# Kernel optimization log

Measured on AMD Instinct MI355X. Metric: run time of the kernel, lower is better.

Reference implementation:

```python
import jax, jax.numpy as jnp
import numpy as np

S, D, H, FF = 2048, 1024, 16, 4096
DH = D // H
EPS = 1e-5


def gelu(x):
    return 0.5 * x * (1 + jnp.tanh(jnp.sqrt(2 / jnp.pi) * (x + 0.044715 * jnp.power(x, 3))))


def layer_norm(x, w, b):
    mu = jnp.mean(x, axis=-1, keepdims=True)
    var = jnp.mean(jnp.square(x - mu), axis=-1, keepdims=True)
    return (x - mu) * jnp.power(var + EPS, -0.5) * w + b


def glorot(key, shape):
    fan_in, fan_out = shape[0], shape[1]
    lim = jnp.sqrt(6.0 / (fan_in + fan_out))
    return jax.random.uniform(key, shape, jnp.float32, -lim, lim)


def setup_inputs() -> dict:
    key = jax.random.key(0)
    ks = jax.random.split(key, 6)
    return {
        "x": jax.random.normal(ks[0], (S, D), jnp.float32),
        "W_qkv": glorot(ks[1], (D, 3 * D)),
        "W_o": glorot(ks[2], (D, D)),
        "W1": glorot(ks[3], (D, FF)),
        "b1": jnp.zeros((FF,), jnp.float32),
        "W2": glorot(ks[4], (FF, D)),
        "b2": jnp.zeros((D,), jnp.float32),
        "ln_att_w": jnp.ones((D,), jnp.float32),
        "ln_att_b": jnp.zeros((D,), jnp.float32),
        "ln_mlp_w": jnp.ones((D,), jnp.float32),
        "ln_mlp_b": jnp.zeros((D,), jnp.float32),
    }


def attention(x, W_qkv, W_o):
    qkv = (x @ W_qkv).reshape(S, 3, H, DH)
    q, k, v = qkv[:, 0], qkv[:, 1], qkv[:, 2]  # each [S, H, DH]
    # scores [H, S_q, S_k]
    scores = jnp.einsum("qhd,khd->hqk", q, k) / jnp.sqrt(jnp.float32(DH))
    causal = jnp.tril(jnp.ones((S, S), bool))
    scores = jnp.where(causal[None], scores, -jnp.inf)
    w = jax.nn.softmax(scores, axis=2)
    out = jnp.einsum("hqk,khd->qhd", w, v).reshape(S, D)
    return out @ W_o


def reference(x, W_qkv, W_o, W1, b1, W2, b2, ln_att_w, ln_att_b, ln_mlp_w, ln_mlp_b):
    x = x + attention(layer_norm(x, ln_att_w, ln_att_b), W_qkv, W_o)
    h = layer_norm(x, ln_mlp_w, ln_mlp_b)
    mlp_out = gelu(h @ W1 + b1) @ W2 + b2
    return x + mlp_out
```

## Files before the change

### kernel.cpp

```cpp
#include <hip/hip_runtime.h>
#include <math.h>

typedef __bf16 bf16;
typedef __bf16 bf16x4 __attribute__((ext_vector_type(4)));
typedef __bf16 bf16x8 __attribute__((ext_vector_type(8)));
typedef float f32x4 __attribute__((ext_vector_type(4)));
typedef unsigned short u16;
typedef unsigned short u16x8 __attribute__((ext_vector_type(8)));
typedef unsigned int u32;

__device__ __forceinline__ u16 f2bf(float f) {
  union { float f; u32 u; } v; v.f = f;
  u32 u = v.u;
  return (u16)((u + 0x7FFFu + ((u >> 16) & 1u)) >> 16);
}

__device__ __forceinline__ f32x4 mfma16(bf16x8 a, bf16x8 b, f32x4 c) {
  return __builtin_amdgcn_mfma_f32_16x16x32_bf16(a, b, c, 0, 0, 0);
}

__device__ __forceinline__ void gld16(const void* g, void* l) {
  __builtin_amdgcn_global_load_lds(
      (const __attribute__((address_space(1))) void*)(void*)g,
      (__attribute__((address_space(3))) void*)l,
      16, 0, 0);
}

__device__ __forceinline__ void wconv_body(const float* __restrict__ W,
                                           u16* __restrict__ Wt, int K, int N,
                                           int bx, int by) {
  __shared__ float tile[64][65];
  const int k0 = by * 64, n0 = bx * 64;
  const int t = threadIdx.x;
  const int tr = t >> 4;
  const int tc = (t & 15) * 4;
#pragma unroll
  for (int it = 0; it < 4; it++) {
    const int r = tr + it * 16;
    const float4 v = *(const float4*)(W + (size_t)(k0 + r) * N + n0 + tc);
    tile[r][tc] = v.x; tile[r][tc + 1] = v.y; tile[r][tc + 2] = v.z; tile[r][tc + 3] = v.w;
  }
  __syncthreads();
#pragma unroll
  for (int it = 0; it < 4; it++) {
    const int rn = tr + it * 16;
    ushort4 o;
    o.x = f2bf(tile[tc][rn]);
    o.y = f2bf(tile[tc + 1][rn]);
    o.z = f2bf(tile[tc + 2][rn]);
    o.w = f2bf(tile[tc + 3][rn]);
    *(ushort4*)(Wt + (size_t)(n0 + rn) * K + k0 + tc) = o;
  }
}

__global__ __launch_bounds__(256)
void wconv_all(const float* __restrict__ Wqkv, const float* __restrict__ Wo,
               const float* __restrict__ W1, const float* __restrict__ W2,
               u16* __restrict__ Wqkv_t, u16* __restrict__ Wo_t,
               u16* __restrict__ W1_t, u16* __restrict__ W2_t) {
  const int id = blockIdx.x;
  if (id < 768)       { wconv_body(Wqkv, Wqkv_t, 1024, 3072, id % 48, id / 48); }
  else if (id < 1024) { const int j = id - 768;  wconv_body(Wo, Wo_t, 1024, 1024, j % 16, j / 16); }
  else if (id < 2048) { const int j = id - 1024; wconv_body(W1, W1_t, 1024, 4096, j % 64, j / 64); }
  else                { const int j = id - 2048; wconv_body(W2, W2_t, 4096, 1024, j % 16, j / 16); }
}

__global__ __launch_bounds__(256)
void ln_bf16(const float* __restrict__ x, const float* __restrict__ w,
             const float* __restrict__ b, u16* __restrict__ out) {
  const int row = blockIdx.x;
  const int t = threadIdx.x;
  const float4 v = *(const float4*)(x + (size_t)row * 1024 + t * 4);
  float s = v.x + v.y + v.z + v.w;
  float s2 = v.x * v.x + v.y * v.y + v.z * v.z + v.w * v.w;
#pragma unroll
  for (int m = 1; m < 64; m <<= 1) {
    s += __shfl_xor(s, m);
    s2 += __shfl_xor(s2, m);
  }
  __shared__ float red[8];
  if ((t & 63) == 0) { red[t >> 6] = s; red[4 + (t >> 6)] = s2; }
  __syncthreads();
  s = red[0] + red[1] + red[2] + red[3];
  s2 = red[4] + red[5] + red[6] + red[7];
  const float mu = s * (1.f / 1024.f);
  const float var = fmaxf(s2 * (1.f / 1024.f) - mu * mu, 0.f);
  const float rstd = rsqrtf(var + 1e-5f);
  const float* wp = w + t * 4;
  const float* bp = b + t * 4;
  ushort4 o;
  o.x = f2bf((v.x - mu) * rstd * wp[0] + bp[0]);
  o.y = f2bf((v.y - mu) * rstd * wp[1] + bp[1]);
  o.z = f2bf((v.z - mu) * rstd * wp[2] + bp[2]);
  o.w = f2bf((v.w - mu) * rstd * wp[3] + bp[3]);
  *(ushort4*)(out + (size_t)row * 1024 + t * 4) = o;
}

__global__ __launch_bounds__(256)
void reduce_ln(const float* __restrict__ x, const float* __restrict__ p0,
               const float* __restrict__ p1, const float* __restrict__ w,
               const float* __restrict__ b, float* __restrict__ x2,
               u16* __restrict__ h2) {
  const int row = blockIdx.x;
  const int t = threadIdx.x;
  const size_t base = (size_t)row * 1024 + t * 4;
  float4 v = *(const float4*)(x + base);
  const float4 a = *(const float4*)(p0 + base);
  const float4 c = *(const float4*)(p1 + base);
  v.x += a.x + c.x; v.y += a.y + c.y; v.z += a.z + c.z; v.w += a.w + c.w;
  *(float4*)(x2 + base) = v;
  float s = v.x + v.y + v.z + v.w;
  float s2 = v.x * v.x + v.y * v.y + v.z * v.z + v.w * v.w;
#pragma unroll
  for (int m = 1; m < 64; m <<= 1) {
    s += __shfl_xor(s, m);
    s2 += __shfl_xor(s2, m);
  }
  __shared__ float red[8];
  if ((t & 63) == 0) { red[t >> 6] = s; red[4 + (t >> 6)] = s2; }
  __syncthreads();
  s = red[0] + red[1] + red[2] + red[3];
  s2 = red[4] + red[5] + red[6] + red[7];
  const float mu = s * (1.f / 1024.f);
  const float var = fmaxf(s2 * (1.f / 1024.f) - mu * mu, 0.f);
  const float rstd = rsqrtf(var + 1e-5f);
  const float* wp = w + t * 4;
  const float* bp = b + t * 4;
  ushort4 o;
  o.x = f2bf((v.x - mu) * rstd * wp[0] + bp[0]);
  o.y = f2bf((v.y - mu) * rstd * wp[1] + bp[1]);
  o.z = f2bf((v.z - mu) * rstd * wp[2] + bp[2]);
  o.w = f2bf((v.w - mu) * rstd * wp[3] + bp[3]);
  *(ushort4*)(h2 + base) = o;
}

__global__ __launch_bounds__(256)
void reduce_out(const float* __restrict__ x2, const float* __restrict__ bias,
                const float* __restrict__ p0, const float* __restrict__ p1,
                float* __restrict__ out) {
  const size_t base = ((size_t)blockIdx.x * 256 + threadIdx.x) * 4;
  const int col = (int)(base & 1023);
  float4 v = *(const float4*)(x2 + base);
  const float4 a = *(const float4*)(p0 + base);
  const float4 c = *(const float4*)(p1 + base);
  const float4 bb = *(const float4*)(bias + col);
  v.x += a.x + c.x + bb.x;
  v.y += a.y + c.y + bb.y;
  v.z += a.z + c.z + bb.z;
  v.w += a.w + c.w + bb.w;
  *(float4*)(out + base) = v;
}

template <int BM, int BN, int EPI, int KS>
__global__ __launch_bounds__(256)
void gemm_bf16(const u16* __restrict__ A, const u16* __restrict__ Bt,
               int M, int N, int K,
               const float* __restrict__ bias,
               float* __restrict__ po0, float* __restrict__ po1,
               u16* __restrict__ outB,
               u16* __restrict__ qo, u16* __restrict__ ko, u16* __restrict__ vo) {
  constexpr int ASZ = BM * 32;
  constexpr int BSZ = BN * 32;
  constexpr int NLD = (BM == 128 ? 2 : 1) + (BN == 128 ? 2 : 1);
  __shared__ __attribute__((aligned(16))) u16 lA[2 * ASZ];
  __shared__ __attribute__((aligned(16))) u16 lB[2 * BSZ];
  const int t = threadIdx.x;
  const int l = t & 63;
  const int w = t >> 6;
  constexpr int NJ = (BM == 128 && BN == 128) ? 4 : 2;
  const int WR = (BM == 128) ? (w >> 1) * 64 : 0;
  const int WC = (BM == 128) ? ((BN == 128) ? (w & 1) * 64 : (w & 1) * 32)
                             : w * 32;
  const int l15 = l & 15, lg = l >> 4;

  const int nx = gridDim.x;
  const u32 bid = blockIdx.y * nx + blockIdx.x;
  const int nxc = nx >> 3;
  const u32 r = bid >> 3;
  const int bx = (bid & 7) * nxc + (int)(r % (u32)nxc);
  const int by = (int)(r / (u32)nxc);

  const int m0 = by * BM, n0 = bx * BN;
  const int KC = K / KS;
  const int kbase = blockIdx.z * KC;

  f32x4 acc[4][NJ] = {};

  const int lr = t >> 2;
  const int lc = ((t & 3) << 3) + kbase;
  const u16* ag0 = A + (size_t)(m0 + lr) * K + lc;
  const u16* ag1 = A + (size_t)(m0 + 64 + lr) * K + lc;
  const u16* bg0 = Bt + (size_t)(n0 + lr) * K + lc;
  const u16* bg1 = Bt + (size_t)(n0 + 64 + lr) * K + lc;

  const int nt = KC / 32;
  auto stage = [&](int buf, int kt) {
    const int k0 = kt * 32;
    gld16(ag0 + k0, &lA[buf * ASZ + t * 8]);
    if (BM == 128) gld16(ag1 + k0, &lA[buf * ASZ + 2048 + t * 8]);
    gld16(bg0 + k0, &lB[buf * BSZ + t * 8]);
    if (BN == 128) gld16(bg1 + k0, &lB[buf * BSZ + 2048 + t * 8]);
  };

  stage(0, 0);

  for (int kt = 0; kt < nt; kt++) {
    const int cur = kt & 1;
    if (kt + 1 < nt) {
      stage(cur ^ 1, kt + 1);
      if constexpr (NLD == 4) {
        asm volatile("s_waitcnt vmcnt(4)" ::: "memory");
      } else {
        asm volatile("s_waitcnt vmcnt(3)" ::: "memory");
      }
    } else {
      asm volatile("s_waitcnt vmcnt(0)" ::: "memory");
    }
    __builtin_amdgcn_s_barrier();
    bf16x8 af[4], bfr[NJ];
#pragma unroll
    for (int i = 0; i < 4; i++)
      af[i] = *(const bf16x8*)&lA[cur * ASZ + (WR + i * 16 + l15) * 32 + lg * 8];
#pragma unroll
    for (int j = 0; j < NJ; j++)
      bfr[j] = *(const bf16x8*)&lB[cur * BSZ + (WC + j * 16 + l15) * 32 + lg * 8];
    asm volatile("s_waitcnt lgkmcnt(0)" ::: "memory");
    __builtin_amdgcn_s_barrier();
    __builtin_amdgcn_sched_barrier(0);
#pragma unroll
    for (int i = 0; i < 4; i++)
#pragma unroll
      for (int j = 0; j < NJ; j++)
        acc[i][j] = mfma16(af[i], bfr[j], acc[i][j]);
  }

  float* po = (KS == 2 && blockIdx.z == 1) ? po1 : po0;
  const int mr0 = m0 + WR + lg * 4;
  const int nc0 = n0 + WC + l15;
#pragma unroll
  for (int i = 0; i < 4; i++) {
    const int mr = mr0 + i * 16;
#pragma unroll
    for (int j = 0; j < NJ; j++) {
      const int nc = nc0 + j * 16;
      if (EPI == 0) {
        const int sel = nc >> 10;
        const int d = nc & 1023;
        const int h = d >> 6, dl = d & 63;
        const int kt2 = mr >> 5;
        if (sel == 2) {
          const int lgp = (mr >> 3) & 3, el0 = mr & 7;
          const int nb = dl >> 4, l15p = dl & 15;
          u16* dst = vo + (size_t)(h * 64 + kt2) * 2048 + nb * 512 +
                     (lgp * 16 + l15p) * 8 + el0;
          ushort4 o;
          o.x = f2bf(acc[i][j][0]); o.y = f2bf(acc[i][j][1]);
          o.z = f2bf(acc[i][j][2]); o.w = f2bf(acc[i][j][3]);
          *(ushort4*)dst = o;
        } else {
          const int f = (mr >> 4) & 1, l15p0 = mr & 15;
          const int kk = dl >> 5, lgp = (dl >> 3) & 3, el = dl & 7;
          u16* dst = (sel == 0 ? qo : ko) + (size_t)(h * 64 + kt2) * 2048 +
                     f * 1024 + kk * 512 + (lgp * 16 + l15p0) * 8 + el;
#pragma unroll
          for (int e = 0; e < 4; e++)
            dst[e * 8] = f2bf(acc[i][j][e]);
        }
      } else if (EPI == 2) {
        const float bb = bias[nc];
#pragma unroll
        for (int e = 0; e < 4; e++) {
          const float v = acc[i][j][e] + bb;
          const float g = 0.5f * v * (1.0f + tanhf(0.7978845608028654f * (v + 0.044715f * v * v * v)));
          outB[(size_t)(mr + e) * N + nc] = f2bf(g);
        }
      } else {
#pragma unroll
        for (int e = 0; e < 4; e++)
          po[(size_t)(mr + e) * N + nc] = acc[i][j][e];
      }
    }
  }
}

__device__ __forceinline__ void attn_load(
    bf16x8 (&kf)[2][2], bf16x8 (&vf)[4],
    const u16* __restrict__ Kp, const u16* __restrict__ Vp,
    int hkt, int l) {
#pragma unroll
  for (int f = 0; f < 2; f++)
#pragma unroll
    for (int kk = 0; kk < 2; kk++)
      kf[kk][f] = *(const bf16x8*)(Kp + hkt + f * 1024 + kk * 512 + l * 8);
#pragma unroll
  for (int nb = 0; nb < 4; nb++)
    vf[nb] = *(const bf16x8*)(Vp + hkt + nb * 512 + l * 8);
}

__device__ __forceinline__ void attn_tile(
    const bf16x8 (&kf)[2][2], const bf16x8 (&vf)[4], const bf16x8 (&qf)[2][2],
    f32x4 (&accO)[2][4], float (&lsum)[2], u16* myP,
    int k0, bool diag, int qb, int l15, int lg) {
  f32x4 sv[2][2] = {};
  __builtin_amdgcn_s_setprio(1);
#pragma unroll
  for (int g = 0; g < 2; g++)
#pragma unroll
    for (int f = 0; f < 2; f++)
#pragma unroll
      for (int kk = 0; kk < 2; kk++)
        sv[g][f] = mfma16(kf[kk][f], qf[g][kk], sv[g][f]);
  __builtin_amdgcn_s_setprio(0);
#pragma unroll
  for (int g = 0; g < 2; g++) {
#pragma unroll
    for (int f = 0; f < 2; f++) {
      bf16x4 pk;
      float ps = 0.f;
#pragma unroll
      for (int e = 0; e < 4; e++) {
        float p = exp2f(sv[g][f][e] * 0.1803368801f);
        if (diag && (k0 + f * 16 + lg * 4 + e > qb + g * 16 + l15)) p = 0.f;
        ps += p;
        pk[e] = (bf16)p;
      }
      lsum[g] += ps;
      *(bf16x4*)(myP + g * 640 + l15 * 40 + f * 16 + lg * 4) = pk;
    }
  }
  const bf16x8 pf0 = *(const bf16x8*)(myP + l15 * 40 + lg * 8);
  const bf16x8 pf1 = *(const bf16x8*)(myP + 640 + l15 * 40 + lg * 8);
  __builtin_amdgcn_s_setprio(1);
#pragma unroll
  for (int nb = 0; nb < 4; nb++) {
    accO[0][nb] = mfma16(pf0, vf[nb], accO[0][nb]);
    accO[1][nb] = mfma16(pf1, vf[nb], accO[1][nb]);
  }
  __builtin_amdgcn_s_setprio(0);
}

__global__ __launch_bounds__(256)
void attn_fwd(const u16* __restrict__ Qp, const u16* __restrict__ Kp,
              const u16* __restrict__ Vp, u16* __restrict__ Ob) {
  __shared__ __attribute__((aligned(16))) char smem[33280];
  float* sO = (float*)smem;
  float* sL = (float*)(smem + 32768);
  u16* lP = (u16*)smem;

  const int t = threadIdx.x;
  const int l = t & 63, w = t >> 6;
  const int l15 = l & 15, lg = l >> 4;
  const u32 bid = blockIdx.x;
  const u32 vb = (bid & 7) * 128 + (bid >> 3);
  const int h = (int)(vb >> 6);
  const int qt = 63 - (int)(vb & 63);
  const int qb = qt * 32;

  u16* myPA = lP + w * 1280;
  u16* myPB = lP + 5120 + w * 1280;

  bf16x8 qf[2][2];
#pragma unroll
  for (int g = 0; g < 2; g++)
#pragma unroll
    for (int kk = 0; kk < 2; kk++)
      qf[g][kk] = *(const bf16x8*)(Qp + (size_t)(h * 64 + qt) * 2048 +
                                   g * 1024 + kk * 512 + l * 8);

  f32x4 accO[2][4] = {};
  float lsum[2] = {0.f, 0.f};

  if (w <= qt) {
    const int hb = h * 64;
    bf16x8 kfA[2][2], vfA[4], kfB[2][2], vfB[4];
    attn_load(kfA, vfA, Kp, Vp, (hb + w) * 2048, l);
    int kt = w;
    while (true) {
      const int ktB = kt + 4;
      const bool hasB = (ktB <= qt);
      attn_load(kfB, vfB, Kp, Vp, (hb + (hasB ? ktB : kt)) * 2048, l);
      attn_tile(kfA, vfA, qf, accO, lsum, myPA, kt * 32, kt == qt, qb, l15, lg);
      if (!hasB) break;
      const int ktA = kt + 8;
      const bool hasA = (ktA <= qt);
      attn_load(kfA, vfA, Kp, Vp, (hb + (hasA ? ktA : ktB)) * 2048, l);
      attn_tile(kfB, vfB, qf, accO, lsum, myPB, ktB * 32, ktB == qt, qb, l15, lg);
      if (!hasA) break;
      kt = ktA;
    }
  }

  float lsr[2];
#pragma unroll
  for (int g = 0; g < 2; g++) {
    float v = lsum[g];
    v += __shfl_xor(v, 16);
    v += __shfl_xor(v, 32);
    lsr[g] = v;
  }

  __syncthreads();
#pragma unroll
  for (int g = 0; g < 2; g++) {
#pragma unroll
    for (int nb = 0; nb < 4; nb++)
#pragma unroll
      for (int e = 0; e < 4; e++)
        sO[w * 2048 + (g * 16 + lg * 4 + e) * 64 + nb * 16 + l15] = accO[g][nb][e];
    if (lg == 0) sL[w * 32 + g * 16 + l15] = lsr[g];
  }
  __syncthreads();

  const int base = t * 8;
  const int row = base >> 6;
  const int col = base & 63;
  f32x4 a0 = {}, a1 = {};
  float ls = 0.f;
#pragma unroll
  for (int ww = 0; ww < 4; ww++) {
    a0 += *(const f32x4*)&sO[ww * 2048 + base];
    a1 += *(const f32x4*)&sO[ww * 2048 + base + 4];
    ls += sL[ww * 32 + row];
  }
  const float rinv = 1.0f / ls;
  u16x8 o;
#pragma unroll
  for (int j = 0; j < 4; j++) {
    o[j] = f2bf(a0[j] * rinv);
    o[4 + j] = f2bf(a1[j] * rinv);
  }
  *(u16x8*)(Ob + (size_t)(qb + row) * 1024 + h * 64 + col) = o;
}

extern "C" void kernel_launch(void* const* d_in, const int* in_sizes, int n_in,
                              void* d_out, int out_size, void* d_ws, size_t ws_size,
                              hipStream_t stream) {
  const float* x     = (const float*)d_in[0];
  const float* W_qkv = (const float*)d_in[1];
  const float* W_o   = (const float*)d_in[2];
  const float* W1    = (const float*)d_in[3];
  const float* b1    = (const float*)d_in[4];
  const float* W2    = (const float*)d_in[5];
  const float* b2    = (const float*)d_in[6];
  const float* ln_aw = (const float*)d_in[7];
  const float* ln_ab = (const float*)d_in[8];
  const float* ln_mw = (const float*)d_in[9];
  const float* ln_mb = (const float*)d_in[10];

  char* ws = (char*)d_ws;
  u16* Wqkv_t = (u16*)(ws);
  u16* Wo_t   = (u16*)(ws + 6291456);
  u16* W1_t   = (u16*)(ws + 8388608);
  u16* W2_t   = (u16*)(ws + 16777216);
  u16* h1     = (u16*)(ws + 25165824);
  u16* h2     = h1;
  u16* Qp     = (u16*)(ws + 29360128);
  u16* Kp     = (u16*)(ws + 33554432);
  u16* Vp     = (u16*)(ws + 37748736);
  u16* attnb  = (u16*)(ws + 41943040);
  u16* ffb    = (u16*)(ws + 29360128);
  float* p0   = (float*)(ws + 46137344);
  float* p1   = (float*)(ws + 54525952);
  float* x2   = (float*)(ws + 62914560);
  (void)ws_size; (void)in_sizes; (void)n_in; (void)out_size;

  wconv_all<<<3072, 256, 0, stream>>>(W_qkv, W_o, W1, W2, Wqkv_t, Wo_t, W1_t, W2_t);

  ln_bf16<<<2048, 256, 0, stream>>>(x, ln_aw, ln_ab, h1);

  gemm_bf16<128, 128, 0, 1><<<dim3(24, 16), 256, 0, stream>>>(
      h1, Wqkv_t, 2048, 3072, 1024, nullptr, nullptr, nullptr, nullptr, Qp, Kp, Vp);

  attn_fwd<<<1024, 256, 0, stream>>>(Qp, Kp, Vp, attnb);

  gemm_bf16<64, 128, 4, 2><<<dim3(8, 32, 2), 256, 0, stream>>>(
      attnb, Wo_t, 2048, 1024, 1024, nullptr, p0, p1, nullptr, nullptr, nullptr, nullptr);

  reduce_ln<<<2048, 256, 0, stream>>>(x, p0, p1, ln_mw, ln_mb, x2, h2);

  gemm_bf16<128, 128, 2, 1><<<dim3(32, 16), 256, 0, stream>>>(
      h2, W1_t, 2048, 4096, 1024, b1, nullptr, nullptr, ffb, nullptr, nullptr, nullptr);

  gemm_bf16<64, 128, 4, 2><<<dim3(8, 32, 2), 256, 0, stream>>>(
      ffb, W2_t, 2048, 1024, 4096, nullptr, p0, p1, nullptr, nullptr, nullptr, nullptr);

  reduce_out<<<2048, 256, 0, stream>>>(x2, b2, p0, p1, (float*)d_out);
}
```

Before: 169.9 us.

## Deepen GEMM pipeline to a 4-slot LDS ring with register-double-buffered fragments

The bf16 GEMM main loop now uses a 4-slot shared-memory ring and prefetches global tiles two K-steps ahead instead of one. The MFMA operand fragments for the next step are loaded from LDS into a second register set while the current step's MFMAs run. This removes the second per-iteration barrier and the full lgkmcnt(0) stall before the MFMAs, so LDS reads and global loads can overlap with compute. In exchange it doubles LDS use per block, which may lower occupancy, and it adds fragment registers. The manual two-step unroll assumes an even number of K tiles.

```diff
diff --git a/kernel.cpp b/kernel.cpp
--- a/kernel.cpp
+++ b/kernel.cpp
@@ -162,12 +162,13 @@
   constexpr int ASZ = BM * 32;
   constexpr int BSZ = BN * 32;
   constexpr int NLD = (BM == 128 ? 2 : 1) + (BN == 128 ? 2 : 1);
-  __shared__ __attribute__((aligned(16))) u16 lA[2 * ASZ];
-  __shared__ __attribute__((aligned(16))) u16 lB[2 * BSZ];
+  constexpr int NJ = (BM == 128 && BN == 128) ? 4 : 2;
+  constexpr int NFR = 4 + NJ;
+  __shared__ __attribute__((aligned(16))) u16 lA[4 * ASZ];
+  __shared__ __attribute__((aligned(16))) u16 lB[4 * BSZ];
   const int t = threadIdx.x;
   const int l = t & 63;
   const int w = t >> 6;
-  constexpr int NJ = (BM == 128 && BN == 128) ? 4 : 2;
   const int WR = (BM == 128) ? (w >> 1) * 64 : 0;
   const int WC = (BM == 128) ? ((BN == 128) ? (w & 1) * 64 : (w & 1) * 32)
                              : w * 32;
@@ -201,37 +202,50 @@
     gld16(bg0 + k0, &lB[buf * BSZ + t * 8]);
     if (BN == 128) gld16(bg1 + k0, &lB[buf * BSZ + 2048 + t * 8]);
   };
-
-  stage(0, 0);
-
-  for (int kt = 0; kt < nt; kt++) {
-    const int cur = kt & 1;
-    if (kt + 1 < nt) {
-      stage(cur ^ 1, kt + 1);
-      if constexpr (NLD == 4) {
-        asm volatile("s_waitcnt vmcnt(4)" ::: "memory");
-      } else {
-        asm volatile("s_waitcnt vmcnt(3)" ::: "memory");
-      }
+  auto ldfrag = [&](int buf, bf16x8 (&af)[4], bf16x8 (&bf_)[NJ]) {
+#pragma unroll
+    for (int i = 0; i < 4; i++)
+      af[i] = *(const bf16x8*)&lA[buf * ASZ + (WR + i * 16 + l15) * 32 + lg * 8];
+#pragma unroll
+    for (int j = 0; j < NJ; j++)
+      bf_[j] = *(const bf16x8*)&lB[buf * BSZ + (WC + j * 16 + l15) * 32 + lg * 8];
+  };
+  auto body = [&](int ti, bf16x8 (&afc)[4], bf16x8 (&bfc)[NJ],
+                  bf16x8 (&afn)[4], bf16x8 (&bfn)[NJ]) {
+    if (ti + 2 < nt) {
+      stage((ti + 2) & 3, ti + 2);
+      if constexpr (NLD == 4) asm volatile("s_waitcnt vmcnt(4)" ::: "memory");
+      else                    asm volatile("s_waitcnt vmcnt(3)" ::: "memory");
     } else {
       asm volatile("s_waitcnt vmcnt(0)" ::: "memory");
     }
     __builtin_amdgcn_s_barrier();
-    bf16x8 af[4], bfr[NJ];
+    if (ti + 1 < nt) {
+      ldfrag((ti + 1) & 3, afn, bfn);
+      if constexpr (NFR == 8) asm volatile("s_waitcnt lgkmcnt(8)" ::: "memory");
+      else                    asm volatile("s_waitcnt lgkmcnt(6)" ::: "memory");
+    } else {
+      asm volatile("s_waitcnt lgkmcnt(0)" ::: "memory");
+    }
+    __builtin_amdgcn_sched_barrier(0);
 #pragma unroll
     for (int i = 0; i < 4; i++)
-      af[i] = *(const bf16x8*)&lA[cur * ASZ + (WR + i * 16 + l15) * 32 + lg * 8];
-#pragma unroll
-    for (int j = 0; j < NJ; j++)
-      bfr[j] = *(const bf16x8*)&lB[cur * BSZ + (WC + j * 16 + l15) * 32 + lg * 8];
-    asm volatile("s_waitcnt lgkmcnt(0)" ::: "memory");
-    __builtin_amdgcn_s_barrier();
-    __builtin_amdgcn_sched_barrier(0);
-#pragma unroll
-    for (int i = 0; i < 4; i++)
 #pragma unroll
       for (int j = 0; j < NJ; j++)
-        acc[i][j] = mfma16(af[i], bfr[j], acc[i][j]);
+        acc[i][j] = mfma16(afc[i], bfc[j], acc[i][j]);
+  };
+
+  stage(0, 0);
+  stage(1, 1);
+  if constexpr (NLD == 4) asm volatile("s_waitcnt vmcnt(4)" ::: "memory");
+  else                    asm volatile("s_waitcnt vmcnt(3)" ::: "memory");
+  __builtin_amdgcn_s_barrier();
+  bf16x8 afA[4], bfA[NJ], afB[4], bfB[NJ];
+  ldfrag(0, afA, bfA);
+
+  for (int ti = 0; ti < nt; ti += 2) {
+    body(ti, afA, bfA, afB, bfB);
+    body(ti + 1, afB, bfB, afA, bfA);
   }
 
   float* po = (KS == 2 && blockIdx.z == 1) ? po1 : po0;
```

Result: no change. 167.6 us (-1.4%).

## Pre-pack GEMM operands into MFMA fragment layout and load directly to registers

Applied to the files above, without the earlier changes.

All bf16 GEMM operands (weights, LN outputs, attention output, GELU output) are now written in a packed 16x32 fragment-tiled layout. The GEMM kernel then loads MFMA fragments straight from global memory into registers with register double-buffering, dropping the LDS staging and barriers. Wo and W2 GEMMs move to 128x128 tiles with split-K of 4, and their partial sums are stored as bf16 instead of fp32 to cut reduction traffic. This adds precision loss in the partials and relies on L2/cache for operand reuse, since there is no shared-memory reuse across waves.

```diff
diff --git a/kernel.cpp b/kernel.cpp
--- a/kernel.cpp
+++ b/kernel.cpp
@@ -14,16 +14,18 @@
   u32 u = v.u;
   return (u16)((u + 0x7FFFu + ((u >> 16) & 1u)) >> 16);
 }
+__device__ __forceinline__ float bf2f(u16 u) {
+  union { u32 u; float f; } v; v.u = (u32)u << 16;
+  return v.f;
+}
 
 __device__ __forceinline__ f32x4 mfma16(bf16x8 a, bf16x8 b, f32x4 c) {
   return __builtin_amdgcn_mfma_f32_16x16x32_bf16(a, b, c, 0, 0, 0);
 }
 
-__device__ __forceinline__ void gld16(const void* g, void* l) {
-  __builtin_amdgcn_global_load_lds(
-      (const __attribute__((address_space(1))) void*)(void*)g,
-      (__attribute__((address_space(3))) void*)l,
-      16, 0, 0);
+__device__ __forceinline__ size_t pk_addr(int r, int c, int C) {
+  return ((size_t)(r >> 4) * (C >> 5) + (c >> 5)) * 512 +
+         ((c >> 3) & 3) * 128 + (r & 15) * 8 + (c & 7);
 }
 
 __device__ __forceinline__ void wconv_body(const float* __restrict__ W,
@@ -44,12 +46,14 @@
 #pragma unroll
   for (int it = 0; it < 4; it++) {
     const int rn = tr + it * 16;
+    const int n = n0 + rn;
+    const int k = k0 + tc;
     ushort4 o;
     o.x = f2bf(tile[tc][rn]);
     o.y = f2bf(tile[tc + 1][rn]);
     o.z = f2bf(tile[tc + 2][rn]);
     o.w = f2bf(tile[tc + 3][rn]);
-    *(ushort4*)(Wt + (size_t)(n0 + rn) * K + k0 + tc) = o;
+    *(ushort4*)(Wt + pk_addr(n, k, K)) = o;
   }
 }
 
@@ -93,21 +97,22 @@
   o.y = f2bf((v.y - mu) * rstd * wp[1] + bp[1]);
   o.z = f2bf((v.z - mu) * rstd * wp[2] + bp[2]);
   o.w = f2bf((v.w - mu) * rstd * wp[3] + bp[3]);
-  *(ushort4*)(out + (size_t)row * 1024 + t * 4) = o;
-}
-
-__global__ __launch_bounds__(256)
-void reduce_ln(const float* __restrict__ x, const float* __restrict__ p0,
-               const float* __restrict__ p1, const float* __restrict__ w,
-               const float* __restrict__ b, float* __restrict__ x2,
-               u16* __restrict__ h2) {
+  *(ushort4*)(out + pk_addr(row, t * 4, 1024)) = o;
+}
+
+__global__ __launch_bounds__(256)
+void reduce_ln(const float* __restrict__ x, const u16* __restrict__ pb,
+               const float* __restrict__ w, const float* __restrict__ b,
+               float* __restrict__ x2, u16* __restrict__ h2) {
   const int row = blockIdx.x;
   const int t = threadIdx.x;
   const size_t base = (size_t)row * 1024 + t * 4;
   float4 v = *(const float4*)(x + base);
-  const float4 a = *(const float4*)(p0 + base);
-  const float4 c = *(const float4*)(p1 + base);
-  v.x += a.x + c.x; v.y += a.y + c.y; v.z += a.z + c.z; v.w += a.w + c.w;
+#pragma unroll
+  for (int z = 0; z < 4; z++) {
+    const ushort4 p = *(const ushort4*)(pb + (size_t)z * 2097152 + base);
+    v.x += bf2f(p.x); v.y += bf2f(p.y); v.z += bf2f(p.z); v.w += bf2f(p.w);
+  }
   *(float4*)(x2 + base) = v;
   float s = v.x + v.y + v.z + v.w;
   float s2 = v.x * v.x + v.y * v.y + v.z * v.z + v.w * v.w;
@@ -131,46 +136,36 @@
   o.y = f2bf((v.y - mu) * rstd * wp[1] + bp[1]);
   o.z = f2bf((v.z - mu) * rstd * wp[2] + bp[2]);
   o.w = f2bf((v.w - mu) * rstd * wp[3] + bp[3]);
-  *(ushort4*)(h2 + base) = o;
+  *(ushort4*)(h2 + pk_addr(row, t * 4, 1024)) = o;
 }
 
 __global__ __launch_bounds__(256)
 void reduce_out(const float* __restrict__ x2, const float* __restrict__ bias,
-                const float* __restrict__ p0, const float* __restrict__ p1,
-                float* __restrict__ out) {
+                const u16* __restrict__ pb, float* __restrict__ out) {
   const size_t base = ((size_t)blockIdx.x * 256 + threadIdx.x) * 4;
   const int col = (int)(base & 1023);
   float4 v = *(const float4*)(x2 + base);
-  const float4 a = *(const float4*)(p0 + base);
-  const float4 c = *(const float4*)(p1 + base);
   const float4 bb = *(const float4*)(bias + col);
-  v.x += a.x + c.x + bb.x;
-  v.y += a.y + c.y + bb.y;
-  v.z += a.z + c.z + bb.z;
-  v.w += a.w + c.w + bb.w;
+  v.x += bb.x; v.y += bb.y; v.z += bb.z; v.w += bb.w;
+#pragma unroll
+  for (int z = 0; z < 4; z++) {
+    const ushort4 p = *(const ushort4*)(pb + (size_t)z * 2097152 + base);
+    v.x += bf2f(p.x); v.y += bf2f(p.y); v.z += bf2f(p.z); v.w += bf2f(p.w);
+  }
   *(float4*)(out + base) = v;
 }
 
-template <int BM, int BN, int EPI, int KS>
-__global__ __launch_bounds__(256)
-void gemm_bf16(const u16* __restrict__ A, const u16* __restrict__ Bt,
-               int M, int N, int K,
-               const float* __restrict__ bias,
-               float* __restrict__ po0, float* __restrict__ po1,
-               u16* __restrict__ outB,
-               u16* __restrict__ qo, u16* __restrict__ ko, u16* __restrict__ vo) {
-  constexpr int ASZ = BM * 32;
-  constexpr int BSZ = BN * 32;
-  constexpr int NLD = (BM == 128 ? 2 : 1) + (BN == 128 ? 2 : 1);
-  __shared__ __attribute__((aligned(16))) u16 lA[2 * ASZ];
-  __shared__ __attribute__((aligned(16))) u16 lB[2 * BSZ];
+template <int EPI, int KS>
+__global__ __launch_bounds__(256)
+void gemm_pk(const u16* __restrict__ Ap, const u16* __restrict__ Bp,
+             int M, int N, int K,
+             const float* __restrict__ bias, u16* __restrict__ pb,
+             u16* __restrict__ outB,
+             u16* __restrict__ qo, u16* __restrict__ ko, u16* __restrict__ vo) {
   const int t = threadIdx.x;
   const int l = t & 63;
   const int w = t >> 6;
-  constexpr int NJ = (BM == 128 && BN == 128) ? 4 : 2;
-  const int WR = (BM == 128) ? (w >> 1) * 64 : 0;
-  const int WC = (BM == 128) ? ((BN == 128) ? (w & 1) * 64 : (w & 1) * 32)
-                             : w * 32;
+  const int WR = (w >> 1) * 64, WC = (w & 1) * 64;
   const int l15 = l & 15, lg = l >> 4;
 
   const int nx = gridDim.x;
@@ -180,68 +175,50 @@
   const int bx = (bid & 7) * nxc + (int)(r % (u32)nxc);
   const int by = (int)(r / (u32)nxc);
 
-  const int m0 = by * BM, n0 = bx * BN;
-  const int KC = K / KS;
-  const int kbase = blockIdx.z * KC;
-
-  f32x4 acc[4][NJ] = {};
-
-  const int lr = t >> 2;
-  const int lc = ((t & 3) << 3) + kbase;
-  const u16* ag0 = A + (size_t)(m0 + lr) * K + lc;
-  const u16* ag1 = A + (size_t)(m0 + 64 + lr) * K + lc;
-  const u16* bg0 = Bt + (size_t)(n0 + lr) * K + lc;
-  const u16* bg1 = Bt + (size_t)(n0 + 64 + lr) * K + lc;
-
-  const int nt = KC / 32;
-  auto stage = [&](int buf, int kt) {
-    const int k0 = kt * 32;
-    gld16(ag0 + k0, &lA[buf * ASZ + t * 8]);
-    if (BM == 128) gld16(ag1 + k0, &lA[buf * ASZ + 2048 + t * 8]);
-    gld16(bg0 + k0, &lB[buf * BSZ + t * 8]);
-    if (BN == 128) gld16(bg1 + k0, &lB[buf * BSZ + 2048 + t * 8]);
+  const int m0 = by * 128, n0 = bx * 128;
+  const int KT = K >> 5;
+  const int nt = (K / KS) >> 5;
+  const int t0 = blockIdx.z * nt;
+
+  const u16* aB = Ap + ((size_t)((m0 + WR) >> 4) * KT + t0) * 512 + l * 8;
+  const u16* bB = Bp + ((size_t)((n0 + WC) >> 4) * KT + t0) * 512 + l * 8;
+
+  f32x4 acc[4][4] = {};
+  bf16x8 a0[4], b0[4], a1[4], b1[4];
+
+  auto LD = [&](bf16x8 (&af)[4], bf16x8 (&bf_)[4], int ti) {
+#pragma unroll
+    for (int i = 0; i < 4; i++)
+      af[i] = *(const bf16x8*)(aB + ((size_t)i * KT + ti) * 512);
+#pragma unroll
+    for (int j = 0; j < 4; j++)
+      bf_[j] = *(const bf16x8*)(bB + ((size_t)j * KT + ti) * 512);
   };
-
-  stage(0, 0);
-
-  for (int kt = 0; kt < nt; kt++) {
-    const int cur = kt & 1;
-    if (kt + 1 < nt) {
-      stage(cur ^ 1, kt + 1);
-      if constexpr (NLD == 4) {
-        asm volatile("s_waitcnt vmcnt(4)" ::: "memory");
-      } else {
-        asm volatile("s_waitcnt vmcnt(3)" ::: "memory");
-      }
-    } else {
-      asm volatile("s_waitcnt vmcnt(0)" ::: "memory");
-    }
-    __builtin_amdgcn_s_barrier();
-    bf16x8 af[4], bfr[NJ];
+  auto FMA = [&](bf16x8 (&af)[4], bf16x8 (&bf_)[4]) {
+    __builtin_amdgcn_s_setprio(1);
 #pragma unroll
     for (int i = 0; i < 4; i++)
-      af[i] = *(const bf16x8*)&lA[cur * ASZ + (WR + i * 16 + l15) * 32 + lg * 8];
-#pragma unroll
-    for (int j = 0; j < NJ; j++)
-      bfr[j] = *(const bf16x8*)&lB[cur * BSZ + (WC + j * 16 + l15) * 32 + lg * 8];
-    asm volatile("s_waitcnt lgkmcnt(0)" ::: "memory");
-    __builtin_amdgcn_s_barrier();
-    __builtin_amdgcn_sched_barrier(0);
-#pragma unroll
-    for (int i = 0; i < 4; i++)
-#pragma unroll
-      for (int j = 0; j < NJ; j++)
-        acc[i][j] = mfma16(af[i], bfr[j], acc[i][j]);
-  }
-
-  float* po = (KS == 2 && blockIdx.z == 1) ? po1 : po0;
+#pragma unroll
+      for (int j = 0; j < 4; j++)
+        acc[i][j] = mfma16(af[i], bf_[j], acc[i][j]);
+    __builtin_amdgcn_s_setprio(0);
+  };
+
+  LD(a0, b0, 0);
+  for (int ti = 0; ti < nt; ti += 2) {
+    LD(a1, b1, (ti + 1 < nt) ? ti + 1 : ti);
+    FMA(a0, b0);
+    LD(a0, b0, (ti + 2 < nt) ? ti + 2 : ti);
+    FMA(a1, b1);
+  }
+
   const int mr0 = m0 + WR + lg * 4;
   const int nc0 = n0 + WC + l15;
 #pragma unroll
   for (int i = 0; i < 4; i++) {
     const int mr = mr0 + i * 16;
 #pragma unroll
-    for (int j = 0; j < NJ; j++) {
+    for (int j = 0; j < 4; j++) {
       const int nc = nc0 + j * 16;
       if (EPI == 0) {
         const int sel = nc >> 10;
@@ -272,12 +249,13 @@
         for (int e = 0; e < 4; e++) {
           const float v = acc[i][j][e] + bb;
           const float g = 0.5f * v * (1.0f + tanhf(0.7978845608028654f * (v + 0.044715f * v * v * v)));
-          outB[(size_t)(mr + e) * N + nc] = f2bf(g);
+          outB[pk_addr(mr + e, nc, 4096)] = f2bf(g);
         }
       } else {
+        u16* po = pb + (size_t)blockIdx.z * M * N;
 #pragma unroll
         for (int e = 0; e < 4; e++)
-          po[(size_t)(mr + e) * N + nc] = acc[i][j][e];
+          po[(size_t)(mr + e) * N + nc] = f2bf(acc[i][j][e]);
       }
     }
   }
@@ -429,7 +407,9 @@
     o[j] = f2bf(a0[j] * rinv);
     o[4 + j] = f2bf(a1[j] * rinv);
   }
-  *(u16x8*)(Ob + (size_t)(qb + row) * 1024 + h * 64 + col) = o;
+  const int grow = qb + row;
+  const int gcol = h * 64 + col;
+  *(u16x8*)(Ob + pk_addr(grow, gcol, 1024)) = o;
 }
 
 extern "C" void kernel_launch(void* const* d_in, const int* in_sizes, int n_in,
@@ -459,8 +439,7 @@
   u16* Vp     = (u16*)(ws + 37748736);
   u16* attnb  = (u16*)(ws + 41943040);
   u16* ffb    = (u16*)(ws + 29360128);
-  float* p0   = (float*)(ws + 46137344);
-  float* p1   = (float*)(ws + 54525952);
+  u16* pb     = (u16*)(ws + 46137344);
   float* x2   = (float*)(ws + 62914560);
   (void)ws_size; (void)in_sizes; (void)n_in; (void)out_size;
 
@@ -468,21 +447,21 @@
 
   ln_bf16<<<2048, 256, 0, stream>>>(x, ln_aw, ln_ab, h1);
 
-  gemm_bf16<128, 128, 0, 1><<<dim3(24, 16), 256, 0, stream>>>(
-      h1, Wqkv_t, 2048, 3072, 1024, nullptr, nullptr, nullptr, nullptr, Qp, Kp, Vp);
+  gemm_pk<0, 1><<<dim3(24, 16), 256, 0, stream>>>(
+      h1, Wqkv_t, 2048, 3072, 1024, nullptr, nullptr, nullptr, Qp, Kp, Vp);
 
   attn_fwd<<<1024, 256, 0, stream>>>(Qp, Kp, Vp, attnb);
 
-  gemm_bf16<64, 128, 4, 2><<<dim3(8, 32, 2), 256, 0, stream>>>(
-      attnb, Wo_t, 2048, 1024, 1024, nullptr, p0, p1, nullptr, nullptr, nullptr, nullptr);
-
-  reduce_ln<<<2048, 256, 0, stream>>>(x, p0, p1, ln_mw, ln_mb, x2, h2);
-
-  gemm_bf16<128, 128, 2, 1><<<dim3(32, 16), 256, 0, stream>>>(
-      h2, W1_t, 2048, 4096, 1024, b1, nullptr, nullptr, ffb, nullptr, nullptr, nullptr);
-
-  gemm_bf16<64, 128, 4, 2><<<dim3(8, 32, 2), 256, 0, stream>>>(
-      ffb, W2_t, 2048, 1024, 4096, nullptr, p0, p1, nullptr, nullptr, nullptr, nullptr);
-
-  reduce_out<<<2048, 256, 0, stream>>>(x2, b2, p0, p1, (float*)d_out);
-}
+  gemm_pk<4, 4><<<dim3(8, 16, 4), 256, 0, stream>>>(
+      attnb, Wo_t, 2048, 1024, 1024, nullptr, pb, nullptr, nullptr, nullptr, nullptr);
+
+  reduce_ln<<<2048, 256, 0, stream>>>(x, pb, ln_mw, ln_mb, x2, h2);
+
+  gemm_pk<2, 1><<<dim3(32, 16), 256, 0, stream>>>(
+      h2, W1_t, 2048, 4096, 1024, b1, nullptr, ffb, nullptr, nullptr, nullptr);
+
+  gemm_pk<4, 4><<<dim3(8, 16, 4), 256, 0, stream>>>(
+      ffb, W2_t, 2048, 1024, 4096, nullptr, pb, nullptr, nullptr, nullptr, nullptr);
+
+  reduce_out<<<2048, 256, 0, stream>>>(x2, b2, pb, (float*)d_out);
+}
```

Result: faster. 151.4 us (-10.9%).
